# Performance work log

Measured on AMD Instinct MI355X. Metric: run time of the kernel, lower is better.

## Reference

```python
import jax, jax.numpy as jnp
import numpy as np

M = 0.25      # margin m
GAMMA = 64.0  # scale gamma
N, D = 8192, 128
NUM_CLASSES = 512


def setup_inputs() -> dict:
    key = jax.random.key(0)
    k1, k2 = jax.random.split(key)
    inputs = jax.random.normal(k1, (N, D), dtype=jnp.float32)
    targets = jax.random.randint(k2, (N,), 0, NUM_CLASSES, dtype=jnp.int64)
    return {"inputs": inputs, "targets": targets}


def reference(inputs, targets):
    # L2-normalize rows -> cosine similarity matrix [n, n]
    x = inputs / jnp.linalg.norm(inputs, axis=1, keepdims=True)
    sim = x @ x.T
    # positive mask: same label (includes diagonal, matching the torch code)
    mask = targets[:, None] == targets[None, :]

    Op, On = 1.0 + M, -M
    delta_p, delta_n = 1.0 - M, M

    sim_d = jax.lax.stop_gradient(sim)  # .detach() in torch
    ap = jnp.maximum(Op - sim_d, 0.0)
    an = jnp.maximum(sim_d + On, 0.0)

    logit_p = -ap * (sim - delta_p) * GAMMA
    logit_n = an * (sim - delta_n) * GAMMA

    neg_inf = jnp.float32(-jnp.inf)
    # per-row logsumexp over positives of -logit_p, over negatives of logit_n
    lp = jax.nn.logsumexp(jnp.where(mask, -logit_p, neg_inf), axis=1)
    ln = jax.nn.logsumexp(jnp.where(mask, neg_inf, logit_n), axis=1)

    return jnp.mean(jax.nn.softplus(ln + lp))
```

## Files before the change

kernel.cpp:

```cpp
#include <hip/hip_runtime.h>
#include <math.h>


#define NR    8192
#define DIMK  128
#define NT    64
#define NBLKS 512
#define NCLS  512
#define MAXC  120

#define CE1 9.6089795f
#define CE0 -2.4022449f

typedef __attribute__((ext_vector_type(8))) short short8;
typedef __attribute__((ext_vector_type(4))) float f32x4;
typedef __attribute__((address_space(3))) uint32_t lds_u32;
typedef const __attribute__((address_space(1))) uint32_t glb_u32;

__device__ __forceinline__ unsigned short bf16_rne(float f) {
  uint32_t u = __float_as_uint(f);
  u += 0x7FFFu + ((u >> 16) & 1u);
  return (unsigned short)(u >> 16);
}

__device__ __forceinline__ float fexp2(float x) {
#if __has_builtin(__builtin_amdgcn_exp2f)
  return __builtin_amdgcn_exp2f(x);
#else
  return exp2f(x);
#endif
}


__global__ __launch_bounds__(256) void normalize_split_kernel(
    const float* __restrict__ x, const int* __restrict__ tgt,
    unsigned short* __restrict__ xhi, unsigned short* __restrict__ xlo,
    float* __restrict__ gP, float* __restrict__ gN,
    int* __restrict__ cnt, int* __restrict__ idx, int* __restrict__ counter) {
  if (blockIdx.x < 32)      gP[blockIdx.x * 256 + threadIdx.x] = 0.f;
  else if (blockIdx.x < 64) gN[(blockIdx.x - 32) * 256 + threadIdx.x] = 0.f;
  if (blockIdx.x == 64 && threadIdx.x == 0) *counter = 0;

  const int wave = threadIdx.x >> 6;
  const int lane = threadIdx.x & 63;
  const int row  = blockIdx.x * 4 + wave;

  if (lane == 0) {
    const int t = tgt[row];
    const int slot = atomicAdd(&cnt[t], 1);
    if (slot < MAXC) idx[t * MAXC + slot] = row;
  }

  const float2 v = ((const float2*)(x + (size_t)row * DIMK))[lane];
  float ss = v.x * v.x + v.y * v.y;
  #pragma unroll
  for (int s = 1; s < 64; s <<= 1) ss += __shfl_xor(ss, s);
  const float r = rsqrtf(ss);
  const float a = v.x * r, b = v.y * r;
  const unsigned short ha = bf16_rne(a), hb = bf16_rne(b);
  const float haf = __uint_as_float((uint32_t)ha << 16);
  const float hbf = __uint_as_float((uint32_t)hb << 16);
  ushort2 hi, lo;
  hi.x = ha; hi.y = hb;
  lo.x = bf16_rne(a - haf); lo.y = bf16_rne(b - hbf);
  ((ushort2*)xhi)[(size_t)row * 64 + lane] = hi;
  ((ushort2*)xlo)[(size_t)row * 64 + lane] = lo;
}

__global__ __launch_bounds__(512, 2) void simloss_kernel(
    const unsigned short* __restrict__ xhi, const unsigned short* __restrict__ xlo,
    const int* __restrict__ cnt, const int* __restrict__ idx,
    float* __restrict__ gP, float* __restrict__ gN,
    int* __restrict__ counter, float* __restrict__ out) {
  __shared__ unsigned short S[32768];
  __shared__ float colbuf[2][4][128];
  __shared__ float red[512];
  __shared__ int midx[MAXC];
  __shared__ int islast;

  const int tid  = threadIdx.x;
  const int wave = tid >> 6, lane = tid & 63;
  const int wy = wave & 3, wx = wave >> 2;
  const int q = lane >> 4, mcol = lane & 15;
  const bool isStage = (wy == 1) || (wy == 2);
  const bool isFlush = (wy == 0);
  const int srank = (wy - 1) + wx * 2;

  {
    float* Sf = (float*)S;
    const int cn = cnt[blockIdx.x];
    const int m  = (cn < MAXC) ? cn : MAXC;
    if (tid < m) midx[tid] = idx[blockIdx.x * MAXC + tid];
    __syncthreads();
    for (int v = tid; v < m * 128; v += 512) {
      const int r = v >> 7, d = v & 127;
      const int row = midx[r];
      const float hi = __uint_as_float((uint32_t)xhi[(size_t)row * DIMK + d] << 16);
      const float lo = __uint_as_float((uint32_t)xlo[(size_t)row * DIMK + d] << 16);
      Sf[r * 129 + d] = hi + lo;
    }
    __syncthreads();
    for (int pr = tid; pr < m * m; pr += 512) {
      const int i = pr / m, j = pr - i * m;
      const float* vi = &Sf[i * 129];
      const float* vj = &Sf[j * 129];
      float s = 0.f;
      #pragma unroll 8
      for (int d = 0; d < 128; ++d) s = fmaf(vi[d], vj[d], s);
      const int gi = midx[i];
      const float ep = __expf(fmaxf(1.25f - s, 0.f) * fmaf(s, 64.f, -48.f));
      atomicAdd(&gP[gi], ep);
      if (i != j) {
        const float u = fmaxf(fmaf(s, CE1, CE0), 0.f);
        atomicAdd(&gN[gi], -fexp2(u * u));
      }
    }
    __syncthreads();
  }

  const int p  = blockIdx.x >> 4;
  const int b  = blockIdx.x & 15;
  const int n1 = NT - p;
  const int t0 = (b * (NT + 1)) >> 4;
  const int t1 = ((b + 1) * (NT + 1)) >> 4;
  const int ntile = t1 - t0;
  const int p2 = NT - 1 - p;

  int cur_bi = (t0 < n1) ? p : p2;

  auto stageA = [&](int bi) {
    const unsigned short* gh = xhi + (size_t)bi * 128 * DIMK;
    const unsigned short* gl = xlo + (size_t)bi * 128 * DIMK;
    #pragma unroll
    for (int g = 0; g < 4; ++g) {
      const int r  = wave * 16 + g * 4 + (lane >> 4);
      const int sc = (lane & 15) ^ (r & 15);
      __builtin_amdgcn_global_load_lds((glb_u32*)(gh + (size_t)r * DIMK + sc * 8),
          (lds_u32*)&S[(wave * 16 + g * 4) * 128], 16, 0, 0);
      __builtin_amdgcn_global_load_lds((glb_u32*)(gl + (size_t)r * DIMK + sc * 8),
          (lds_u32*)&S[16384 + (wave * 16 + g * 4) * 128], 16, 0, 0);
    }
  };
  auto stageB = [&](int bj, int buf) {
    const unsigned short* gb = xhi + (size_t)bj * 128 * DIMK;
    unsigned short* dst = &S[buf * 16384];
    #pragma unroll
    for (int g = 0; g < 8; ++g) {
      const int r  = srank * 32 + g * 4 + (lane >> 4);
      const int sc = (lane & 15) ^ (r & 15);
      __builtin_amdgcn_global_load_lds((glb_u32*)(gb + (size_t)r * DIMK + sc * 8),
          (lds_u32*)&dst[(srank * 32 + g * 4) * 128], 16, 0, 0);
    }
  };

  short8 Ah[2][4], Al[2][4];
  auto extractA = [&]() {
    #pragma unroll
    for (int fr = 0; fr < 2; ++fr) {
      const int r = wy * 32 + fr * 16 + mcol;
      #pragma unroll
      for (int ks = 0; ks < 4; ++ks) {
        const int pc = (ks * 4 + q) ^ mcol;
        Ah[fr][ks] = *(const short8*)&S[r * 128 + pc * 8];
        Al[fr][ks] = *(const short8*)&S[16384 + r * 128 + pc * 8];
      }
    }
  };

  float rowN[2][4] = {{0.f}};
  auto flushRows = [&](int bi_) {
    #pragma unroll
    for (int fr = 0; fr < 2; ++fr)
      #pragma unroll
      for (int rg = 0; rg < 4; ++rg) {
        float vn = rowN[fr][rg];
        #pragma unroll
        for (int m2 = 1; m2 < 16; m2 <<= 1) vn += __shfl_xor(vn, m2);
        if (mcol == 0)
          atomicAdd(&gN[bi_ * 128 + wy * 32 + fr * 16 + q * 4 + rg], vn);
      }
  };

  stageA(cur_bi);
  __syncthreads();
  extractA();
  __builtin_amdgcn_s_waitcnt(49279);
  __builtin_amdgcn_s_barrier();
  if (isStage) stageB((t0 < n1) ? p + t0 : p2 + (t0 - n1), 0);

  for (int tl = 0; tl < ntile; ++tl) {
    const int ix = t0 + tl;
    const int bi = (ix < n1) ? p : p2;
    const int bj = (ix < n1) ? p + ix : p2 + (ix - n1);

    if (bi != cur_bi) {
      flushRows(cur_bi);
      cur_bi = bi;
      stageA(cur_bi);
      __syncthreads();
      extractA();
      #pragma unroll
      for (int fr = 0; fr < 2; ++fr)
        #pragma unroll
        for (int rg = 0; rg < 4; ++rg) rowN[fr][rg] = 0.f;
      __builtin_amdgcn_s_waitcnt(49279);
      __builtin_amdgcn_s_barrier();
      if (isStage) stageB(bj, tl & 1);
    }

    if (isStage) __builtin_amdgcn_s_waitcnt(112);
    __builtin_amdgcn_s_barrier();

    if (tl + 1 < ntile) {
      const int ix2 = ix + 1;
      if ((ix2 < n1) == (ix < n1)) {
        const int bj2 = (ix2 < n1) ? p + ix2 : p2 + (ix2 - n1);
        if (isStage) stageB(bj2, (tl + 1) & 1);
      }
    }

    const unsigned short* Bb = &S[(tl & 1) * 16384];
    f32x4 acc[2][4];
    #pragma unroll
    for (int fr = 0; fr < 2; ++fr)
      #pragma unroll
      for (int fc = 0; fc < 4; ++fc)
        acc[fr][fc] = (f32x4){0.f, 0.f, 0.f, 0.f};
    #pragma unroll
    for (int ks = 0; ks < 4; ++ks) {
      short8 bh[4];
      #pragma unroll
      for (int fc = 0; fc < 4; ++fc) {
        const int rb = wx * 64 + fc * 16 + mcol;
        const int pc = (ks * 4 + q) ^ mcol;
        bh[fc] = *(const short8*)&Bb[rb * 128 + pc * 8];
      }
      #pragma unroll
      for (int fc = 0; fc < 4; ++fc) {
        acc[0][fc] = __builtin_amdgcn_mfma_f32_16x16x32_bf16(Ah[0][ks], bh[fc], acc[0][fc], 0, 0, 0);
        acc[1][fc] = __builtin_amdgcn_mfma_f32_16x16x32_bf16(Ah[1][ks], bh[fc], acc[1][fc], 0, 0, 0);
        acc[0][fc] = __builtin_amdgcn_mfma_f32_16x16x32_bf16(Al[0][ks], bh[fc], acc[0][fc], 0, 0, 0);
        acc[1][fc] = __builtin_amdgcn_mfma_f32_16x16x32_bf16(Al[1][ks], bh[fc], acc[1][fc], 0, 0, 0);
      }
    }

    float cN[4] = {0.f, 0.f, 0.f, 0.f};
#define EPILOGUE(DIAG_)                                                      \
    {                                                                        \
      _Pragma("unroll")                                                      \
      for (int fr = 0; fr < 2; ++fr) {                                       \
        _Pragma("unroll")                                                    \
        for (int rg = 0; rg < 4; ++rg) {                                     \
          float vn = 0.f;                                                    \
          _Pragma("unroll")                                                  \
          for (int fc = 0; fc < 4; ++fc) {                                   \
            const float s = acc[fr][fc][rg];                                 \
            const float u = fmaxf(fmaf(s, CE1, CE0), 0.f);                   \
            float e = fexp2(u * u);                                          \
            if (DIAG_) {                                                     \
              const int rl = wy * 32 + fr * 16 + q * 4 + rg;                 \
              const int cl = wx * 64 + fc * 16 + mcol;                       \
              e = (rl == cl) ? 0.f : e;                                      \
            }                                                                \
            vn += e;                                                         \
            cN[fc] += e;                                                     \
          }                                                                  \
          rowN[fr][rg] += vn;                                                \
        }                                                                    \
      }                                                                      \
    }
    if (bj == bi) EPILOGUE(true) else EPILOGUE(false)
#undef EPILOGUE

    #pragma unroll
    for (int fc = 0; fc < 4; ++fc) {
      cN[fc] += __shfl_xor(cN[fc], 16);
      cN[fc] += __shfl_xor(cN[fc], 32);
    }
    if (q == 0) {
      #pragma unroll
      for (int fc = 0; fc < 4; ++fc)
        colbuf[tl & 1][wy][wx * 64 + fc * 16 + mcol] = cN[fc];
    }
    __builtin_amdgcn_s_waitcnt(49279);
    __builtin_amdgcn_s_barrier();

    if (isFlush && bj != bi) {
      const int col = wx * 64 + lane;
      float sn = 0.f;
      #pragma unroll
      for (int w = 0; w < 4; ++w) sn += colbuf[tl & 1][w][col];
      atomicAdd(&gN[bj * 128 + col], sn);
    }
  }
  flushRows(cur_bi);

  __builtin_amdgcn_s_waitcnt(0);
  __syncthreads();
  if (tid == 0) islast = (atomicAdd(counter, 1) == NBLKS - 1) ? 1 : 0;
  __syncthreads();
  if (islast) {
    float local = 0.f;
    #pragma unroll 1
    for (int bb = 0; bb < 2; ++bb) {
      const int base = bb * 4096 + tid * 8;
      float pv[8], nv[8];
      #pragma unroll
      for (int u = 0; u < 8; ++u) pv[u] = atomicAdd(&gP[base + u], 0.0f);
      #pragma unroll
      for (int u = 0; u < 8; ++u) nv[u] = atomicAdd(&gN[base + u], 0.0f);
      #pragma unroll
      for (int u = 0; u < 8; ++u) local += log1pf(pv[u] * nv[u]);
    }
    red[tid] = local;
    __syncthreads();
    for (int s2 = 256; s2 > 0; s2 >>= 1) {
      if (tid < s2) red[tid] += red[tid + s2];
      __syncthreads();
    }
    if (tid == 0) out[0] = red[0] / (float)NR;
  }
}

extern "C" void kernel_launch(void* const* d_in, const int* in_sizes, int n_in,
                              void* d_out, int out_size, void* d_ws, size_t ws_size,
                              hipStream_t stream) {
  const float* x  = (const float*)d_in[0];
  const int* tgt  = (const int*)d_in[1];
  float* out      = (float*)d_out;

  unsigned short* xhi = (unsigned short*)d_ws;
  unsigned short* xlo = xhi + (size_t)NR * DIMK;
  float* gP = (float*)((char*)d_ws + (size_t)NR * DIMK * 4);
  float* gN = gP + NR;
  int* cnt = (int*)(gN + NR);
  int* idx = cnt + NCLS;
  int* counter = idx + NCLS * MAXC;

  hipMemsetAsync(cnt, 0, NCLS * sizeof(int), stream);
  normalize_split_kernel<<<NR / 4, 256, 0, stream>>>(x, tgt, xhi, xlo, gP, gN, cnt, idx, counter);
  simloss_kernel<<<NBLKS, 512, 0, stream>>>(xhi, xlo, cnt, idx, gP, gN, counter, out);
}
```

Baseline: 124.4 us.

## Drop memset and global class buckets; scan labels per block after main loop

Removes the hipMemsetAsync launch and the atomic class-bucket construction in the normalize kernel. Each simloss block now scans all 8192 targets itself to find the rows of its class, and runs the same-class correction at the end of the kernel instead of the beginning. This is meant to cut one launch and the global atomics, and to let the correction sit behind the main tile work rather than delay its start. In exchange every block reads the full target array, the correction now adds to each block's tail, and MAXC grows to 128.

```diff
diff --git a/kernel.cpp b/kernel.cpp
--- a/kernel.cpp
+++ b/kernel.cpp
@@ -6,8 +6,7 @@
 #define DIMK  128
 #define NT    64
 #define NBLKS 512
-#define NCLS  512
-#define MAXC  120
+#define MAXC  128
 
 #define CE1 9.6089795f
 #define CE0 -2.4022449f
@@ -33,10 +32,9 @@
 
 
 __global__ __launch_bounds__(256) void normalize_split_kernel(
-    const float* __restrict__ x, const int* __restrict__ tgt,
-    unsigned short* __restrict__ xhi, unsigned short* __restrict__ xlo,
-    float* __restrict__ gP, float* __restrict__ gN,
-    int* __restrict__ cnt, int* __restrict__ idx, int* __restrict__ counter) {
+    const float* __restrict__ x, unsigned short* __restrict__ xhi,
+    unsigned short* __restrict__ xlo, float* __restrict__ gP,
+    float* __restrict__ gN, int* __restrict__ counter) {
   if (blockIdx.x < 32)      gP[blockIdx.x * 256 + threadIdx.x] = 0.f;
   else if (blockIdx.x < 64) gN[(blockIdx.x - 32) * 256 + threadIdx.x] = 0.f;
   if (blockIdx.x == 64 && threadIdx.x == 0) *counter = 0;
@@ -44,13 +42,6 @@
   const int wave = threadIdx.x >> 6;
   const int lane = threadIdx.x & 63;
   const int row  = blockIdx.x * 4 + wave;
-
-  if (lane == 0) {
-    const int t = tgt[row];
-    const int slot = atomicAdd(&cnt[t], 1);
-    if (slot < MAXC) idx[t * MAXC + slot] = row;
-  }
-
   const float2 v = ((const float2*)(x + (size_t)row * DIMK))[lane];
   float ss = v.x * v.x + v.y * v.y;
   #pragma unroll
@@ -69,13 +60,13 @@
 
 __global__ __launch_bounds__(512, 2) void simloss_kernel(
     const unsigned short* __restrict__ xhi, const unsigned short* __restrict__ xlo,
-    const int* __restrict__ cnt, const int* __restrict__ idx,
-    float* __restrict__ gP, float* __restrict__ gN,
+    const int* __restrict__ tgt, float* __restrict__ gP, float* __restrict__ gN,
     int* __restrict__ counter, float* __restrict__ out) {
   __shared__ unsigned short S[32768];
   __shared__ float colbuf[2][4][128];
   __shared__ float red[512];
   __shared__ int midx[MAXC];
+  __shared__ int scnt;
   __shared__ int islast;
 
   const int tid  = threadIdx.x;
@@ -85,38 +76,6 @@
   const bool isStage = (wy == 1) || (wy == 2);
   const bool isFlush = (wy == 0);
   const int srank = (wy - 1) + wx * 2;
-
-  {
-    float* Sf = (float*)S;
-    const int cn = cnt[blockIdx.x];
-    const int m  = (cn < MAXC) ? cn : MAXC;
-    if (tid < m) midx[tid] = idx[blockIdx.x * MAXC + tid];
-    __syncthreads();
-    for (int v = tid; v < m * 128; v += 512) {
-      const int r = v >> 7, d = v & 127;
-      const int row = midx[r];
-      const float hi = __uint_as_float((uint32_t)xhi[(size_t)row * DIMK + d] << 16);
-      const float lo = __uint_as_float((uint32_t)xlo[(size_t)row * DIMK + d] << 16);
-      Sf[r * 129 + d] = hi + lo;
-    }
-    __syncthreads();
-    for (int pr = tid; pr < m * m; pr += 512) {
-      const int i = pr / m, j = pr - i * m;
-      const float* vi = &Sf[i * 129];
-      const float* vj = &Sf[j * 129];
-      float s = 0.f;
-      #pragma unroll 8
-      for (int d = 0; d < 128; ++d) s = fmaf(vi[d], vj[d], s);
-      const int gi = midx[i];
-      const float ep = __expf(fmaxf(1.25f - s, 0.f) * fmaf(s, 64.f, -48.f));
-      atomicAdd(&gP[gi], ep);
-      if (i != j) {
-        const float u = fmaxf(fmaf(s, CE1, CE0), 0.f);
-        atomicAdd(&gN[gi], -fexp2(u * u));
-      }
-    }
-    __syncthreads();
-  }
 
   const int p  = blockIdx.x >> 4;
   const int b  = blockIdx.x & 15;
@@ -295,6 +254,43 @@
   }
   flushRows(cur_bi);
 
+  {
+    if (tid == 0) scnt = 0;
+    __syncthreads();
+    for (int v = tid; v < NR; v += 512) {
+      if (tgt[v] == (int)blockIdx.x) {
+        const int slot = atomicAdd(&scnt, 1);
+        if (slot < MAXC) midx[slot] = v;
+      }
+    }
+    __syncthreads();
+    const int m = (scnt < MAXC) ? scnt : MAXC;
+    float* Sf = (float*)S;
+    for (int v = tid; v < m * 128; v += 512) {
+      const int r = v >> 7, d = v & 127;
+      const int row = midx[r];
+      const float hi = __uint_as_float((uint32_t)xhi[(size_t)row * DIMK + d] << 16);
+      const float lo = __uint_as_float((uint32_t)xlo[(size_t)row * DIMK + d] << 16);
+      Sf[r * 129 + d] = hi + lo;
+    }
+    __syncthreads();
+    for (int pr = tid; pr < m * m; pr += 512) {
+      const int i = pr / m, j = pr - i * m;
+      const float* vi = &Sf[i * 129];
+      const float* vj = &Sf[j * 129];
+      float s = 0.f;
+      #pragma unroll 8
+      for (int d = 0; d < 128; ++d) s = fmaf(vi[d], vj[d], s);
+      const int gi = midx[i];
+      const float ep = __expf(fmaxf(1.25f - s, 0.f) * fmaf(s, 64.f, -48.f));
+      atomicAdd(&gP[gi], ep);
+      if (i != j) {
+        const float u = fmaxf(fmaf(s, CE1, CE0), 0.f);
+        atomicAdd(&gN[gi], -fexp2(u * u));
+      }
+    }
+  }
+
   __builtin_amdgcn_s_waitcnt(0);
   __syncthreads();
   if (tid == 0) islast = (atomicAdd(counter, 1) == NBLKS - 1) ? 1 : 0;
@@ -333,11 +329,8 @@
   unsigned short* xlo = xhi + (size_t)NR * DIMK;
   float* gP = (float*)((char*)d_ws + (size_t)NR * DIMK * 4);
   float* gN = gP + NR;
-  int* cnt = (int*)(gN + NR);
-  int* idx = cnt + NCLS;
-  int* counter = idx + NCLS * MAXC;
-
-  hipMemsetAsync(cnt, 0, NCLS * sizeof(int), stream);
-  normalize_split_kernel<<<NR / 4, 256, 0, stream>>>(x, tgt, xhi, xlo, gP, gN, cnt, idx, counter);
-  simloss_kernel<<<NBLKS, 512, 0, stream>>>(xhi, xlo, cnt, idx, gP, gN, counter, out);
-}
+  int* counter = (int*)(gN + NR);
+
+  normalize_split_kernel<<<NR / 4, 256, 0, stream>>>(x, xhi, xlo, gP, gN, counter);
+  simloss_kernel<<<NBLKS, 512, 0, stream>>>(xhi, xlo, tgt, gP, gN, counter, out);
+}
```

After: 126.3 us. No clear change (+1.5%).
